# Optimization experiments

Hardware: AMD Instinct MI355X
Metric: run time of the kernel (lower is better)

## Reference

```python
import jax, jax.numpy as jnp
import numpy as np

D_MODEL = 128
N_HEADS = 8
HEAD_DIM = D_MODEL // N_HEADS
N_EXPERTS = 256
B, T = 4, 512


def rmsnorm(x, gamma, eps=1e-6):
    norm = jnp.sqrt(jnp.mean(jnp.square(x), axis=-1, keepdims=True) + eps)
    return gamma * (x / norm)


def apply_rope(x):
    # x: (B, T, H, D) -- half-split (NeoX-style) rotation
    Bx, Tx, Hx, Dx = x.shape
    inv_freq = 1.0 / (10000.0 ** (jnp.arange(0, Dx, 2, dtype=jnp.float32) / Dx))
    t = jnp.arange(Tx, dtype=jnp.float32)
    freqs = jnp.outer(t, inv_freq)                      # (T, D/2)
    sin_f = jnp.sin(freqs)[None, :, None, :]            # (1, T, 1, D/2)
    cos_f = jnp.cos(freqs)[None, :, None, :]
    x1, x2 = jnp.split(x, 2, axis=-1)
    return jnp.concatenate([x1 * cos_f - x2 * sin_f, x1 * sin_f + x2 * cos_f], axis=-1)


def swiglu(x, w1, b1, w2, b2):
    gate = x @ w1 + b1
    return gate * jax.nn.sigmoid(gate) * (x @ w2 + b2)


def lightning_attention(x, wq, bq, wk, bk, wv, bv, wo, bo):
    Bx, Tx, _ = x.shape
    q = (x @ wq + bq).reshape(Bx, Tx, N_HEADS, HEAD_DIM)
    k = (x @ wk + bk).reshape(Bx, Tx, N_HEADS, HEAD_DIM)
    v = (x @ wv + bv).reshape(Bx, Tx, N_HEADS, HEAD_DIM)
    q = jax.nn.elu(apply_rope(q)) + 1.0
    k = jax.nn.elu(apply_rope(k)) + 1.0
    q = q.transpose(0, 2, 1, 3)  # (B,H,T,D)
    k = k.transpose(0, 2, 1, 3)
    v = v.transpose(0, 2, 1, 3)
    ctx = jnp.einsum('bhtd,bhte->bhde', k, v)           # (B,H,D,D)
    out = jnp.einsum('bhtd,bhde->bhte', q, ctx)         # (B,H,T,D)
    k_sum = jnp.sum(k, axis=2)                          # (B,H,D)
    z = 1.0 / (jnp.einsum('bhtd,bhd->bht', q, k_sum) + 1e-6)
    out = out * z[..., None]
    out = out.transpose(0, 2, 1, 3).reshape(Bx, Tx, D_MODEL)
    return out @ wo + bo


def turbo_quant(x, rot, scale):
    y = x @ rot
    mag = jnp.sqrt(jnp.mean(jnp.square(y), axis=-1, keepdims=True) + 1e-6)
    phase = y / mag
    quant = jnp.round(phase * 8.0) / 8.0
    phase = jax.lax.stop_gradient(quant - phase) + phase  # STE
    return phase * mag * scale


def gated_moe(h, gate_w, gate_b, exp_w, mw1, mb1, mw2, mb2):
    gate_scores = jax.nn.softmax(h @ gate_w + gate_b, axis=-1)       # (B,T,E)
    top_vals, top_idx = jax.lax.top_k(gate_scores, 2)                # (B,T,2)
    top_w = top_vals / (jnp.sum(top_vals, axis=-1, keepdims=True) + 1e-6)
    onehot = jax.nn.one_hot(top_idx, N_EXPERTS, dtype=h.dtype)       # (B,T,2,E)
    mask = jnp.sum(onehot * top_w[..., None], axis=2)                # (B,T,E)
    expert_outputs = jnp.einsum('btd,edo->bteo', h, exp_w)           # (B,T,E,D)
    weighted_avg = jnp.einsum('bteo,bte->bto', expert_outputs, mask)
    weighted_avg = swiglu(weighted_avg, mw1, mb1, mw2, mb2)
    diff_sq = jnp.square(expert_outputs - weighted_avg[:, :, None, :])
    weighted_var = jnp.einsum('bteo,bte->bto', diff_sq, mask)
    consensus = jnp.exp(-jnp.mean(weighted_var, axis=-1))            # (B,T)
    return weighted_avg, consensus


def setup_inputs() -> dict:
    key = jax.random.key(0)
    ks = jax.random.split(key, 24)
    d = D_MODEL
    dw = lambda k, shp: (jax.random.normal(k, shp, dtype=jnp.float32) * 0.02)
    rng = np.random.RandomState(42)
    Q, _ = np.linalg.qr(rng.randn(d, d))
    return {
        'x': jax.random.normal(ks[0], (B, T, d), dtype=jnp.float32),
        'g1': jnp.ones((d,), jnp.float32),
        'wq': dw(ks[1], (d, d)), 'bq': jnp.zeros((d,), jnp.float32),
        'wk': dw(ks[2], (d, d)), 'bk': jnp.zeros((d,), jnp.float32),
        'wv': dw(ks[3], (d, d)), 'bv': jnp.zeros((d,), jnp.float32),
        'wo': dw(ks[4], (d, d)), 'bo': jnp.zeros((d,), jnp.float32),
        'rot': jnp.asarray(Q.astype('float32')),
        'tq_scale': jnp.ones((d,), jnp.float32),
        'sw_w1': dw(ks[5], (d, d)), 'sw_b1': jnp.zeros((d,), jnp.float32),
        'sw_w2': dw(ks[6], (d, d)), 'sw_b2': jnp.zeros((d,), jnp.float32),
        'g2': jnp.ones((d,), jnp.float32),
        'gate_w': dw(ks[7], (d, N_EXPERTS)), 'gate_b': jnp.zeros((N_EXPERTS,), jnp.float32),
        'exp_w': dw(ks[8], (N_EXPERTS, d, d)),
        'moe_w1': dw(ks[9], (d, d)), 'moe_b1': jnp.zeros((d,), jnp.float32),
        'moe_w2': dw(ks[10], (d, d)), 'moe_b2': jnp.zeros((d,), jnp.float32),
    }


def reference(x, g1, wq, bq, wk, bk, wv, bv, wo, bo, rot, tq_scale,
              sw_w1, sw_b1, sw_w2, sw_b2, g2, gate_w, gate_b, exp_w,
              moe_w1, moe_b1, moe_w2, moe_b2):
    attn_out = lightning_attention(rmsnorm(x, g1), wq, bq, wk, bk, wv, bv, wo, bo)
    attn_out = turbo_quant(attn_out, rot, tq_scale)
    x = x + swiglu(attn_out, sw_w1, sw_b1, sw_w2, sw_b2)
    moe_out, consensus = gated_moe(rmsnorm(x, g2), gate_w, gate_b, exp_w,
                                   moe_w1, moe_b1, moe_w2, moe_b2)
    x = x + moe_out
    return x, consensus
```

## Files before the change

kernel.cpp:

```cpp
#include <hip/hip_runtime.h>
#include <math.h>

#define DM 128
#define SEQ 512
#define NTOK 2048
#define NH 8
#define HD 16
#define NE 256

__device__ __forceinline__ float sigmoid_f(float v) { return 1.0f / (1.0f + expf(-v)); }

__device__ __forceinline__ float wave_sum64(float v) {
#pragma unroll
  for (int m = 32; m; m >>= 1) v += __shfl_xor(v, m, 64);
  return v;
}

__global__ __launch_bounds__(512) void k_qkv(
    const float* __restrict__ x, const float* __restrict__ g1,
    const float* __restrict__ wq, const float* __restrict__ bq,
    const float* __restrict__ wk, const float* __restrict__ bk,
    const float* __restrict__ wv, const float* __restrict__ bv_,
    float* __restrict__ q, float* __restrict__ k, float* __restrict__ v) {
  const int tid = threadIdx.x;
  const int o = tid & 127, ks = tid >> 7;
  const int n0 = blockIdx.x * 4;
  __shared__ float h1[4][DM];
  __shared__ float qr[4][DM], kr[4][DM];
  __shared__ float red3[4][4][DM][3];
  __shared__ float wredA[8];

  float xv = x[(n0 + ks) * DM + o];
  float s = wave_sum64(xv * xv);
  if ((tid & 63) == 0) wredA[tid >> 6] = s;
  __syncthreads();
  float tot = wredA[2 * ks] + wredA[2 * ks + 1];
  float rinv = 1.0f / sqrtf(tot * (1.0f / 128.0f) + 1e-6f);
  h1[ks][o] = g1[o] * xv * rinv;
  __syncthreads();

  float aq[4] = {0, 0, 0, 0}, ak[4] = {0, 0, 0, 0}, av[4] = {0, 0, 0, 0};
  const int d0 = ks * 32;
  for (int dd = 0; dd < 32; ++dd) {
    int d = d0 + dd;
    float wqv = wq[d * DM + o], wkv = wk[d * DM + o], wvv = wv[d * DM + o];
#pragma unroll
    for (int g = 0; g < 4; ++g) {
      float hv = h1[g][d];
      aq[g] = fmaf(hv, wqv, aq[g]);
      ak[g] = fmaf(hv, wkv, ak[g]);
      av[g] = fmaf(hv, wvv, av[g]);
    }
  }
#pragma unroll
  for (int g = 0; g < 4; ++g) {
    red3[ks][g][o][0] = aq[g];
    red3[ks][g][o][1] = ak[g];
    red3[ks][g][o][2] = av[g];
  }
  __syncthreads();
  float sq = bq[o], sk = bk[o], sv = bv_[o];
#pragma unroll
  for (int s2 = 0; s2 < 4; ++s2) {
    sq += red3[s2][ks][o][0];
    sk += red3[s2][ks][o][1];
    sv += red3[s2][ks][o][2];
  }
  qr[ks][o] = sq;
  kr[ks][o] = sk;
  v[(n0 + ks) * DM + o] = sv;
  __syncthreads();

  const int i = o & 15, j = i & 7, hi = i & 8, lo = o & ~8;
  const float invf = expf(-(float)j * 1.1512925464970229f);
  int t = (n0 + ks) & (SEQ - 1);
  float ang = (float)t * invf;
  float sn = sinf(ang), cs = cosf(ang);
  float x1q = qr[ks][lo], x2q = qr[ks][lo + 8];
  float x1k = kr[ks][lo], x2k = kr[ks][lo + 8];
  float rq = hi ? (x1q * sn + x2q * cs) : (x1q * cs - x2q * sn);
  float rk = hi ? (x1k * sn + x2k * cs) : (x1k * cs - x2k * sn);
  rq = (rq > 0.0f) ? rq + 1.0f : expf(rq);
  rk = (rk > 0.0f) ? rk + 1.0f : expf(rk);
  q[(n0 + ks) * DM + o] = rq;
  k[(n0 + ks) * DM + o] = rk;
}

__global__ __launch_bounds__(256) void k_ctxp(
    const float* __restrict__ k, const float* __restrict__ v,
    float* __restrict__ ctxp, float* __restrict__ ksump) {
  const int bh = blockIdx.x & 31, tc = blockIdx.x >> 5;
  const int b = bh >> 3, h = bh & 7;
  const int p = threadIdx.x, d = p >> 4, e = p & 15;
  const float* kb = k + (size_t)b * SEQ * DM + h * HD;
  const float* vb = v + (size_t)b * SEQ * DM + h * HD;
  float acc = 0.0f, kss = 0.0f;
  for (int tt = 0; tt < 64; ++tt) {
    int t = tc * 64 + tt;
    float kv = kb[t * DM + d];
    float vv = vb[t * DM + e];
    acc = fmaf(kv, vv, acc);
    kss += kv;
  }
  ctxp[tc * 8192 + bh * 256 + p] = acc;
  if (e == 0) ksump[tc * 512 + bh * HD + d] = kss;
}

__global__ __launch_bounds__(512) void k_attn(
    const float* __restrict__ x, const float* __restrict__ qp,
    const float* __restrict__ ctxp, const float* __restrict__ ksump,
    const float* __restrict__ wo, const float* __restrict__ bo,
    const float* __restrict__ rot, const float* __restrict__ tqs,
    const float* __restrict__ w1, const float* __restrict__ b1,
    const float* __restrict__ w2, const float* __restrict__ b2,
    const float* __restrict__ g2,
    float* __restrict__ xmid, float* __restrict__ h2o) {
  const int tid = threadIdx.x;
  const int o = tid & 127, ks = tid >> 7;
  const int n0 = blockIdx.x * 4;
  const int b = n0 >> 9;
  __shared__ float ctxs[NH * 256];
  __shared__ float kss[DM];
  __shared__ float rowA[4][DM], rowB[4][DM];
  __shared__ float red2[4][4][DM][2];
  __shared__ float wredA[8], wredB[8];

  for (int idx = tid; idx < 2048; idx += 512) {
    float s = 0.0f;
#pragma unroll
    for (int tc = 0; tc < 8; ++tc) s += ctxp[tc * 8192 + b * 2048 + idx];
    ctxs[idx] = s;
  }
  if (tid < 128) {
    float s = 0.0f;
#pragma unroll
    for (int tc = 0; tc < 8; ++tc) s += ksump[tc * 512 + b * DM + tid];
    kss[tid] = s;
  }
  rowA[ks][o] = qp[(n0 + ks) * DM + o];
  __syncthreads();

  {
    int h = o >> 4, e = o & 15;
    float oa = 0.0f, qk = 0.0f;
#pragma unroll
    for (int d = 0; d < HD; ++d) {
      float qv = rowA[ks][h * HD + d];
      oa = fmaf(qv, ctxs[h * 256 + d * 16 + e], oa);
      qk = fmaf(qv, kss[h * HD + d], qk);
    }
    rowB[ks][o] = oa / (qk + 1e-6f);
  }
  __syncthreads();

  const int d0 = ks * 32;
  {
    float acc[4] = {0, 0, 0, 0};
    for (int dd = 0; dd < 32; ++dd) {
      int d = d0 + dd;
      float w = wo[d * DM + o];
#pragma unroll
      for (int g = 0; g < 4; ++g) acc[g] = fmaf(rowB[g][d], w, acc[g]);
    }
#pragma unroll
    for (int g = 0; g < 4; ++g) red2[ks][g][o][0] = acc[g];
  }
  __syncthreads();
  {
    float sa = bo[o];
#pragma unroll
    for (int s2 = 0; s2 < 4; ++s2) sa += red2[s2][ks][o][0];
    rowA[ks][o] = sa;
  }
  __syncthreads();

  {
    float acc[4] = {0, 0, 0, 0};
    for (int dd = 0; dd < 32; ++dd) {
      int d = d0 + dd;
      float r = rot[d * DM + o];
#pragma unroll
      for (int g = 0; g < 4; ++g) acc[g] = fmaf(rowA[g][d], r, acc[g]);
    }
#pragma unroll
    for (int g = 0; g < 4; ++g) red2[ks][g][o][1] = acc[g];
  }
  __syncthreads();
  {
    float y = 0.0f;
#pragma unroll
    for (int s2 = 0; s2 < 4; ++s2) y += red2[s2][ks][o][1];
    float ssq = wave_sum64(y * y);
    if ((tid & 63) == 0) wredA[tid >> 6] = ssq;
    __syncthreads();
    float tot = wredA[2 * ks] + wredA[2 * ks + 1];
    float mag = sqrtf(tot * (1.0f / 128.0f) + 1e-6f);
    float phase = y / mag;
    rowB[ks][o] = rintf(phase * 8.0f) * 0.125f * mag * tqs[o];
  }
  __syncthreads();

  {
    float a1[4] = {0, 0, 0, 0}, a2[4] = {0, 0, 0, 0};
    for (int dd = 0; dd < 32; ++dd) {
      int d = d0 + dd;
      float w1v = w1[d * DM + o];
      float w2v = w2[d * DM + o];
#pragma unroll
      for (int g = 0; g < 4; ++g) {
        float t = rowB[g][d];
        a1[g] = fmaf(t, w1v, a1[g]);
        a2[g] = fmaf(t, w2v, a2[g]);
      }
    }
#pragma unroll
    for (int g = 0; g < 4; ++g) {
      red2[ks][g][o][0] = a1[g];
      red2[ks][g][o][1] = a2[g];
    }
  }
  __syncthreads();
  {
    float ga = b1[o], up = b2[o];
#pragma unroll
    for (int s2 = 0; s2 < 4; ++s2) {
      ga += red2[s2][ks][o][0];
      up += red2[s2][ks][o][1];
    }
    float swv = ga * sigmoid_f(ga) * up;
    float xm = x[(n0 + ks) * DM + o] + swv;
    xmid[(n0 + ks) * DM + o] = xm;
    float ssq = wave_sum64(xm * xm);
    if ((tid & 63) == 0) wredB[tid >> 6] = ssq;
    __syncthreads();
    float tot = wredB[2 * ks] + wredB[2 * ks + 1];
    float rinv = 1.0f / sqrtf(tot * (1.0f / 128.0f) + 1e-6f);
    h2o[(n0 + ks) * DM + o] = g2[o] * xm * rinv;
  }
}

__global__ __launch_bounds__(1024) void k_moe(
    const float* __restrict__ h2, const float* __restrict__ xmid,
    const float* __restrict__ gate_w, const float* __restrict__ gate_b,
    const float* __restrict__ exp_w,
    const float* __restrict__ mw1, const float* __restrict__ mb1,
    const float* __restrict__ mw2, const float* __restrict__ mb2,
    float* __restrict__ out_x, float* __restrict__ out_cons) {
  const int tid = threadIdx.x;
  const int n0 = blockIdx.x * 4;
  __shared__ float h2s[4][DM];
  __shared__ float redg[4][4][NE];
  __shared__ float lgl[4][NE];
  __shared__ float el[4][2][DM];
  __shared__ float was[4][DM];
  __shared__ float redm[2][4][DM][2];
  __shared__ int sie[4][2];
  __shared__ float sw[4][2];
  __shared__ float wredV[8];

  if (tid < 512) {
    int g = tid >> 7, o = tid & 127;
    h2s[g][o] = h2[(n0 + g) * DM + o];
  }
  __syncthreads();

  {
    int e = tid & 255, kq = tid >> 8;
    float lg[4] = {0, 0, 0, 0};
    for (int dd = 0; dd < 32; ++dd) {
      int d = kq * 32 + dd;
      float gw = gate_w[d * NE + e];
#pragma unroll
      for (int g = 0; g < 4; ++g) lg[g] = fmaf(h2s[g][d], gw, lg[g]);
    }
#pragma unroll
    for (int g = 0; g < 4; ++g) redg[kq][g][e] = lg[g];
  }
  __syncthreads();
  {
    int e = tid & 255, kq = tid >> 8;
    float lf = gate_b[e];
#pragma unroll
    for (int s2 = 0; s2 < 4; ++s2) lf += redg[s2][kq][e];
    lgl[kq][e] = lf;
  }
  __syncthreads();

  if (tid < 256) {
    int lane = tid & 63, g = tid >> 6;
    float bv = -INFINITY;
    int bi = 0;
#pragma unroll
    for (int j2 = 0; j2 < 4; ++j2) {
      int e = lane + 64 * j2;
      float vv = lgl[g][e];
      if (vv > bv || (vv == bv && e < bi)) { bv = vv; bi = e; }
    }
#pragma unroll
    for (int m = 32; m; m >>= 1) {
      float pv = __shfl_xor(bv, m, 64);
      int pi = __shfl_xor(bi, m, 64);
      if (pv > bv || (pv == bv && pi < bi)) { bv = pv; bi = pi; }
    }
    float se = 0.0f;
#pragma unroll
    for (int j2 = 0; j2 < 4; ++j2) se += expf(lgl[g][lane + 64 * j2] - bv);
    se = wave_sum64(se);
    float mv = -INFINITY;
    int mi = 0;
#pragma unroll
    for (int j2 = 0; j2 < 4; ++j2) {
      int e = lane + 64 * j2;
      if (e != bi) {
        float vv = lgl[g][e];
        if (vv > mv || (vv == mv && e < mi)) { mv = vv; mi = e; }
      }
    }
#pragma unroll
    for (int m = 32; m; m >>= 1) {
      float pv = __shfl_xor(mv, m, 64);
      int pi = __shfl_xor(mi, m, 64);
      if (pv > mv || (pv == mv && pi < mi)) { mv = pv; mi = pi; }
    }
    if (lane == 0) {
      float v0 = 1.0f / se;
      float v1 = expf(mv - bv) / se;
      float wsum = v0 + v1 + 1e-6f;
      sie[g][0] = bi;
      sie[g][1] = mi;
      sw[g][0] = v0 / wsum;
      sw[g][1] = v1 / wsum;
    }
  }
  __syncthreads();

  {
    int asn = tid >> 7, o = tid & 127;
    int g = asn >> 1, slot = asn & 1;
    const float* W = exp_w + (size_t)sie[g][slot] * (DM * DM);
    float ea = 0.0f;
    for (int d = 0; d < DM; ++d) ea = fmaf(h2s[g][d], W[d * DM + o], ea);
    el[g][slot][o] = ea;
  }
  __syncthreads();
  if (tid < 512) {
    int g = tid >> 7, o = tid & 127;
    was[g][o] = sw[g][0] * el[g][0][o] + sw[g][1] * el[g][1][o];
  }
  __syncthreads();

  {
    int kh = tid >> 9, r = tid & 511, g = r >> 7, o = r & 127;
    float a1 = 0.0f, a2 = 0.0f;
    for (int dd = 0; dd < 64; ++dd) {
      int d = kh * 64 + dd;
      float w1v = mw1[d * DM + o];
      float w2v = mw2[d * DM + o];
      float t = was[g][d];
      a1 = fmaf(t, w1v, a1);
      a2 = fmaf(t, w2v, a2);
    }
    redm[kh][g][o][0] = a1;
    redm[kh][g][o][1] = a2;
  }
  __syncthreads();
  if (tid < 512) {
    int g = tid >> 7, o = tid & 127;
    float ga = redm[0][g][o][0] + redm[1][g][o][0] + mb1[o];
    float up = redm[0][g][o][1] + redm[1][g][o][1] + mb2[o];
    float swv = ga * sigmoid_f(ga) * up;
    out_x[(size_t)(n0 + g) * DM + o] = xmid[(size_t)(n0 + g) * DM + o] + swv;
    float dd0 = el[g][0][o] - swv;
    float dd1 = el[g][1][o] - swv;
    float vt = sw[g][0] * dd0 * dd0 + sw[g][1] * dd1 * dd1;
    vt = wave_sum64(vt);
    if ((tid & 63) == 0) wredV[tid >> 6] = vt;
  }
  __syncthreads();
  if (tid < 4)
    out_cons[n0 + tid] = expf(-(wredV[2 * tid] + wredV[2 * tid + 1]) * (1.0f / 128.0f));
}

extern "C" void kernel_launch(void* const* d_in, const int* in_sizes, int n_in,
                              void* d_out, int out_size, void* d_ws, size_t ws_size,
                              hipStream_t stream) {
  const float* x = (const float*)d_in[0];
  const float* g1 = (const float*)d_in[1];
  const float* wq = (const float*)d_in[2];
  const float* bq = (const float*)d_in[3];
  const float* wk = (const float*)d_in[4];
  const float* bk = (const float*)d_in[5];
  const float* wv = (const float*)d_in[6];
  const float* bv = (const float*)d_in[7];
  const float* wo = (const float*)d_in[8];
  const float* bo = (const float*)d_in[9];
  const float* rot = (const float*)d_in[10];
  const float* tqs = (const float*)d_in[11];
  const float* sw1 = (const float*)d_in[12];
  const float* sb1 = (const float*)d_in[13];
  const float* sw2 = (const float*)d_in[14];
  const float* sb2 = (const float*)d_in[15];
  const float* g2 = (const float*)d_in[16];
  const float* gw = (const float*)d_in[17];
  const float* gb = (const float*)d_in[18];
  const float* ew = (const float*)d_in[19];
  const float* mw1 = (const float*)d_in[20];
  const float* mb1 = (const float*)d_in[21];
  const float* mw2 = (const float*)d_in[22];
  const float* mb2 = (const float*)d_in[23];

  float* ws = (float*)d_ws;
  float* q = ws;
  float* k = ws + 262144;
  float* v = ws + 524288;
  float* ctxp = ws + 786432;
  float* ksump = ws + 851968;
  float* xmid = ws + 856064;
  float* h2 = ws + 1118208;
  float* out_x = (float*)d_out;
  float* out_c = out_x + (size_t)NTOK * DM;

  hipLaunchKernelGGL(k_qkv, dim3(NTOK / 4), dim3(512), 0, stream,
                     x, g1, wq, bq, wk, bk, wv, bv, q, k, v);
  hipLaunchKernelGGL(k_ctxp, dim3(256), dim3(256), 0, stream, k, v, ctxp, ksump);
  hipLaunchKernelGGL(k_attn, dim3(NTOK / 4), dim3(512), 0, stream,
                     x, q, ctxp, ksump, wo, bo, rot, tqs, sw1, sb1, sw2, sb2, g2,
                     xmid, h2);
  hipLaunchKernelGGL(k_moe, dim3(NTOK / 4), dim3(1024), 0, stream,
                     h2, xmid, gw, gb, ew, mw1, mb1, mw2, mb2, out_x, out_c);
}
```

Baseline: 67.21 us.

## Group MoE tokens by expert via atomic lists and run per-expert matmul blocks

Splits the fused MoE kernel into gating, per-expert and combine kernels. Gating appends token assignments to per-expert lists with atomics, and the expert kernel holds one expert's weights in registers across all of its assigned tokens. This replaces the old per-token gather of a 64KB expert matrix with one weight read per expert. It adds two kernel launches, a memset and atomics, and load imbalance across experts is possible.

```diff
diff --git a/kernel.cpp b/kernel.cpp
--- a/kernel.cpp
+++ b/kernel.cpp
@@ -7,6 +7,7 @@
 #define NH 8
 #define HD 16
 #define NE 256
+#define CAP 4096
 
 __device__ __forceinline__ float sigmoid_f(float v) { return 1.0f / (1.0f + expf(-v)); }
 
@@ -239,24 +240,15 @@
   }
 }
 
-__global__ __launch_bounds__(1024) void k_moe(
-    const float* __restrict__ h2, const float* __restrict__ xmid,
-    const float* __restrict__ gate_w, const float* __restrict__ gate_b,
-    const float* __restrict__ exp_w,
-    const float* __restrict__ mw1, const float* __restrict__ mb1,
-    const float* __restrict__ mw2, const float* __restrict__ mb2,
-    float* __restrict__ out_x, float* __restrict__ out_cons) {
+__global__ __launch_bounds__(1024) void k_gate(
+    const float* __restrict__ h2, const float* __restrict__ gate_w,
+    const float* __restrict__ gate_b,
+    float* __restrict__ tw, int* __restrict__ cnt, int* __restrict__ list) {
   const int tid = threadIdx.x;
   const int n0 = blockIdx.x * 4;
   __shared__ float h2s[4][DM];
   __shared__ float redg[4][4][NE];
   __shared__ float lgl[4][NE];
-  __shared__ float el[4][2][DM];
-  __shared__ float was[4][DM];
-  __shared__ float redm[2][4][DM][2];
-  __shared__ int sie[4][2];
-  __shared__ float sw[4][2];
-  __shared__ float wredV[8];
 
   if (tid < 512) {
     int g = tid >> 7, o = tid & 127;
@@ -326,59 +318,96 @@
       float v0 = 1.0f / se;
       float v1 = expf(mv - bv) / se;
       float wsum = v0 + v1 + 1e-6f;
-      sie[g][0] = bi;
-      sie[g][1] = mi;
-      sw[g][0] = v0 / wsum;
-      sw[g][1] = v1 / wsum;
-    }
-  }
-  __syncthreads();
-
-  {
-    int asn = tid >> 7, o = tid & 127;
-    int g = asn >> 1, slot = asn & 1;
-    const float* W = exp_w + (size_t)sie[g][slot] * (DM * DM);
-    float ea = 0.0f;
-    for (int d = 0; d < DM; ++d) ea = fmaf(h2s[g][d], W[d * DM + o], ea);
-    el[g][slot][o] = ea;
-  }
-  __syncthreads();
-  if (tid < 512) {
-    int g = tid >> 7, o = tid & 127;
-    was[g][o] = sw[g][0] * el[g][0][o] + sw[g][1] * el[g][1][o];
-  }
-  __syncthreads();
-
-  {
-    int kh = tid >> 9, r = tid & 511, g = r >> 7, o = r & 127;
-    float a1 = 0.0f, a2 = 0.0f;
-    for (int dd = 0; dd < 64; ++dd) {
-      int d = kh * 64 + dd;
-      float w1v = mw1[d * DM + o];
-      float w2v = mw2[d * DM + o];
-      float t = was[g][d];
-      a1 = fmaf(t, w1v, a1);
-      a2 = fmaf(t, w2v, a2);
-    }
-    redm[kh][g][o][0] = a1;
-    redm[kh][g][o][1] = a2;
-  }
-  __syncthreads();
-  if (tid < 512) {
-    int g = tid >> 7, o = tid & 127;
-    float ga = redm[0][g][o][0] + redm[1][g][o][0] + mb1[o];
-    float up = redm[0][g][o][1] + redm[1][g][o][1] + mb2[o];
-    float swv = ga * sigmoid_f(ga) * up;
-    out_x[(size_t)(n0 + g) * DM + o] = xmid[(size_t)(n0 + g) * DM + o] + swv;
-    float dd0 = el[g][0][o] - swv;
-    float dd1 = el[g][1][o] - swv;
-    float vt = sw[g][0] * dd0 * dd0 + sw[g][1] * dd1 * dd1;
-    vt = wave_sum64(vt);
-    if ((tid & 63) == 0) wredV[tid >> 6] = vt;
-  }
+      int t = n0 + g;
+      tw[t * 2 + 0] = v0 / wsum;
+      tw[t * 2 + 1] = v1 / wsum;
+      int r0 = atomicAdd(&cnt[bi], 1);
+      list[bi * CAP + r0] = t * 2 + 0;
+      int r1 = atomicAdd(&cnt[mi], 1);
+      list[mi * CAP + r1] = t * 2 + 1;
+    }
+  }
+}
+
+__global__ __launch_bounds__(512) void k_exp(
+    const float* __restrict__ h2, const float* __restrict__ exp_w,
+    const int* __restrict__ cnt, const int* __restrict__ list,
+    float* __restrict__ elbuf) {
+  const int e = blockIdx.x;
+  const int nt = cnt[e];
+  if (nt == 0) return;
+  const int tid = threadIdx.x;
+  const int o = tid & 127, qq = tid >> 7;
+  const float* W = exp_w + (size_t)e * (DM * DM);
+  float wreg[32];
+#pragma unroll
+  for (int dd = 0; dd < 32; ++dd) wreg[dd] = W[(qq * 32 + dd) * DM + o];
+  __shared__ float h2t[8][DM];
+  __shared__ float psum[4][8][DM];
+  __shared__ int alst[8];
+
+  for (int i0 = 0; i0 < nt; i0 += 8) {
+    int gn = min(8, nt - i0);
+    for (int idx = tid; idx < gn * 128; idx += 512) {
+      int j = idx >> 7;
+      int a = list[e * CAP + i0 + j];
+      h2t[j][idx & 127] = h2[(size_t)(a >> 1) * DM + (idx & 127)];
+    }
+    if (tid < gn) alst[tid] = list[e * CAP + i0 + tid];
+    __syncthreads();
+    for (int j = 0; j < gn; ++j) {
+      const float4* hp = (const float4*)&h2t[j][qq * 32];
+      float acc = 0.0f;
+#pragma unroll
+      for (int d4 = 0; d4 < 8; ++d4) {
+        float4 hv = hp[d4];
+        acc = fmaf(wreg[d4 * 4 + 0], hv.x, acc);
+        acc = fmaf(wreg[d4 * 4 + 1], hv.y, acc);
+        acc = fmaf(wreg[d4 * 4 + 2], hv.z, acc);
+        acc = fmaf(wreg[d4 * 4 + 3], hv.w, acc);
+      }
+      psum[qq][j][o] = acc;
+    }
+    __syncthreads();
+    for (int j = qq; j < gn; j += 4) {
+      float r = psum[0][j][o] + psum[1][j][o] + psum[2][j][o] + psum[3][j][o];
+      elbuf[(size_t)alst[j] * DM + o] = r;
+    }
+    __syncthreads();
+  }
+}
+
+__global__ __launch_bounds__(512) void k_comb(
+    const float* __restrict__ elbuf, const float* __restrict__ tw,
+    const float* __restrict__ xmid,
+    const float* __restrict__ mw1, const float* __restrict__ mb1,
+    const float* __restrict__ mw2, const float* __restrict__ mb2,
+    float* __restrict__ out_x, float* __restrict__ out_cons) {
+  const int tid = threadIdx.x;
+  const int g = tid >> 7, o = tid & 127;
+  const int t = blockIdx.x * 4 + g;
+  __shared__ float was[4][DM];
+  __shared__ float wredV[8];
+  float w0 = tw[t * 2 + 0], w1 = tw[t * 2 + 1];
+  float el0 = elbuf[(size_t)(t * 2 + 0) * DM + o];
+  float el1 = elbuf[(size_t)(t * 2 + 1) * DM + o];
+  was[g][o] = w0 * el0 + w1 * el1;
+  __syncthreads();
+  float a1 = mb1[o], a2 = mb2[o];
+  for (int d = 0; d < DM; ++d) {
+    float tt = was[g][d];
+    a1 = fmaf(tt, mw1[d * DM + o], a1);
+    a2 = fmaf(tt, mw2[d * DM + o], a2);
+  }
+  float swv = a1 * sigmoid_f(a1) * a2;
+  out_x[(size_t)t * DM + o] = xmid[(size_t)t * DM + o] + swv;
+  float dd0 = el0 - swv, dd1 = el1 - swv;
+  float vt = wave_sum64(w0 * dd0 * dd0 + w1 * dd1 * dd1);
+  if ((tid & 63) == 0) wredV[tid >> 6] = vt;
   __syncthreads();
   if (tid < 4)
-    out_cons[n0 + tid] = expf(-(wredV[2 * tid] + wredV[2 * tid + 1]) * (1.0f / 128.0f));
+    out_cons[blockIdx.x * 4 + tid] =
+        expf(-(wredV[2 * tid] + wredV[2 * tid + 1]) * (1.0f / 128.0f));
 }
 
 extern "C" void kernel_launch(void* const* d_in, const int* in_sizes, int n_in,
@@ -417,15 +446,24 @@
   float* ksump = ws + 851968;
   float* xmid = ws + 856064;
   float* h2 = ws + 1118208;
+  float* tw = ws + 1380352;
+  float* elbuf = ws + 1384448;
+  int* cnt = (int*)(ws + 1908736);
+  int* list = (int*)(ws + 1908992);
   float* out_x = (float*)d_out;
   float* out_c = out_x + (size_t)NTOK * DM;
 
+  hipMemsetAsync(cnt, 0, NE * sizeof(int), stream);
   hipLaunchKernelGGL(k_qkv, dim3(NTOK / 4), dim3(512), 0, stream,
                      x, g1, wq, bq, wk, bk, wv, bv, q, k, v);
   hipLaunchKernelGGL(k_ctxp, dim3(256), dim3(256), 0, stream, k, v, ctxp, ksump);
   hipLaunchKernelGGL(k_attn, dim3(NTOK / 4), dim3(512), 0, stream,
                      x, q, ctxp, ksump, wo, bo, rot, tqs, sw1, sb1, sw2, sb2, g2,
                      xmid, h2);
-  hipLaunchKernelGGL(k_moe, dim3(NTOK / 4), dim3(1024), 0, stream,
-                     h2, xmid, gw, gb, ew, mw1, mb1, mw2, mb2, out_x, out_c);
-}
+  hipLaunchKernelGGL(k_gate, dim3(NTOK / 4), dim3(1024), 0, stream,
+                     h2, gw, gb, tw, cnt, list);
+  hipLaunchKernelGGL(k_exp, dim3(NE), dim3(512), 0, stream,
+                     h2, ew, cnt, list, elbuf);
+  hipLaunchKernelGGL(k_comb, dim3(NTOK / 4), dim3(512), 0, stream,
+                     elbuf, tw, xmid, mw1, mb1, mw2, mb2, out_x, out_c);
+}
```

After: 75.34 us. 12.1% more time.
